# Kernel optimization log

Measured on AMD Instinct MI355X. Metric: run time of the kernel, lower is better.

The kernel has to match this reference:

```python
import jax, jax.numpy as jnp
import numpy as np

L, B, S, E, H, V = 2, 64, 64, 1024, 1024, 32000


def _uni(key, shape, k):
    return jax.random.uniform(key, shape, jnp.float32, -k, k)


def setup_inputs() -> dict:
    key = jax.random.key(0)
    ks = jax.random.split(key, 16)
    k = 1.0 / np.sqrt(H)
    inp = {
        "inputs": jax.random.randint(ks[0], (S, B), 0, V),
        "hidden": jnp.zeros((L, B, H), jnp.float32),
        "emb": jax.random.uniform(ks[1], (V, E), jnp.float32, -0.1, 0.1),
        # per-layer GRU weights stacked on leading L axis (layer0 input = emb = H)
        "Wx": _uni(ks[2], (L, H, H), k),   # linear_W (no bias), used for r gate
        "Ur": _uni(ks[3], (L, H, H), k),
        "br": _uni(ks[4], (L, H), k),
        "Wz": _uni(ks[5], (L, H, H), k),
        "Uz": _uni(ks[6], (L, H, H), k),
        "bz": _uni(ks[7], (L, H), k),
        "Wh": _uni(ks[8], (L, H, H), k),
        "Uh": _uni(ks[9], (L, H, H), k),
        "bh": _uni(ks[10], (L, H), k),
        "dec_W": jax.random.uniform(ks[11], (V, H), jnp.float32, -0.1, 0.1),
        "dec_b": jnp.zeros((V,), jnp.float32),
    }
    return inp


def _gru_cell(x, h, Wx, Ur, br, Wz, Uz, bz, Wh, Uh, bh):
    # faithful to GRU_Hidden.forward (r gate uses linear_W, bias-free W projections)
    r = jax.nn.sigmoid(x @ Wx.T + h @ Ur.T + br)
    z = jax.nn.sigmoid(x @ Wz.T + h @ Uz.T + bz)
    h_cand = jnp.tanh(x @ Wh.T + (r * h) @ Uh.T + bh)
    return (1.0 - z) * h + z * h_cand


def reference(inputs, hidden, emb, Wx, Ur, br, Wz, Uz, bz, Wh, Uh, bh, dec_W, dec_b):
    x_embs = emb[inputs]  # [S, B, E]; dropout is identity (dp_keep_prob = 1.0)
    n_layers = Wx.shape[0]

    def step(h, x_t):
        new_h = []
        inp = x_t
        for l in range(n_layers):
            hl = _gru_cell(inp, h[l], Wx[l], Ur[l], br[l], Wz[l], Uz[l], bz[l], Wh[l], Uh[l], bh[l])
            new_h.append(hl)
            inp = hl
        logits_t = inp @ dec_W.T + dec_b  # [B, V]
        return jnp.stack(new_h), logits_t

    h_final, logits = jax.lax.scan(step, hidden, x_embs)
    return logits, h_final
```

## Files before the change

### kernel.cpp

```cpp
#include <hip/hip_runtime.h>

#define SBV 131072000

typedef __bf16 bf16x8 __attribute__((ext_vector_type(8)));
typedef float  f32x4  __attribute__((ext_vector_type(4)));
typedef unsigned short u16;

__device__ __forceinline__ u16 f2bf(float f) {
  union { float f; unsigned u; } c; c.f = f;
  return (u16)((c.u + 0x7fffu + ((c.u >> 16) & 1u)) >> 16);
}
__device__ __forceinline__ float sigm(float x) { return 1.f / (1.f + __expf(-x)); }
__device__ __forceinline__ float tanh_f(float x) { return 2.f / (1.f + __expf(-2.f * x)) - 1.f; }


__global__ void k_cvtv(const float* __restrict__ src, u16* __restrict__ dst, int n4) {
  const float4* s4 = (const float4*)src;
  ushort4* d4 = (ushort4*)dst;
  for (int i = blockIdx.x * blockDim.x + threadIdx.x; i < n4; i += gridDim.x * blockDim.x) {
    float4 v = s4[i];
    ushort4 o; o.x = f2bf(v.x); o.y = f2bf(v.y); o.z = f2bf(v.z); o.w = f2bf(v.w);
    d4[i] = o;
  }
}

__global__ void k_pack3(const float* __restrict__ sx, const float* __restrict__ sz,
                        const float* __restrict__ sh, int srcOff, u16* __restrict__ dst) {
  int i = blockIdx.x * blockDim.x + threadIdx.x;
  if (i >= 786432) return;
  int g = i >> 18;
  int r4 = i & 262143;
  const float* s = (g == 0 ? sx : (g == 1 ? sz : sh)) + srcOff;
  float4 v = ((const float4*)s)[r4];
  ushort4 o; o.x = f2bf(v.x); o.y = f2bf(v.y); o.z = f2bf(v.z); o.w = f2bf(v.w);
  ((ushort4*)dst)[i] = o;
}

__global__ void k_embed(const int* __restrict__ idx, const float* __restrict__ emb,
                        u16* __restrict__ xe) {
  int i = blockIdx.x * blockDim.x + threadIdx.x;
  if (i >= 1048576) return;
  int row = i >> 8, k4 = i & 255;
  int e = idx[row];
  float4 v = ((const float4*)emb)[(size_t)e * 256 + k4];
  ushort4 o; o.x = f2bf(v.x); o.y = f2bf(v.y); o.z = f2bf(v.z); o.w = f2bf(v.w);
  ((ushort4*)xe)[i] = o;
}

__global__ __launch_bounds__(256) void gemm_bt(const u16* __restrict__ A, const u16* __restrict__ Bm,
                                               float* __restrict__ C, int M, int N, int K, int mtiles) {
  __shared__ u16 As[128 * 32];
  __shared__ u16 Bs[128 * 32];
  const int tid = threadIdx.x;
  const int bm = blockIdx.x % mtiles, bn = blockIdx.x / mtiles;
  const int m0 = bm * 128, n0 = bn * 128;
  const int lane = tid & 63, w = tid >> 6, wm = w & 1, wn = w >> 1;
  const int la = lane & 15, lk = lane >> 4;
  const int srow = tid >> 2, sk = (tid & 3) * 8;
  f32x4 acc[4][4] = {};
  for (int kt = 0; kt < K; kt += 32) {
    const u16* srcA0 = A + (size_t)(m0 + srow) * K + kt + sk;
    const u16* srcA1 = A + (size_t)(m0 + srow + 64) * K + kt + sk;
    const u16* srcB0 = Bm + (size_t)(n0 + srow) * K + kt + sk;
    const u16* srcB1 = Bm + (size_t)(n0 + srow + 64) * K + kt + sk;
    __builtin_amdgcn_global_load_lds((const __attribute__((address_space(1))) void*)srcA0,
        (__attribute__((address_space(3))) void*)((char*)As + tid * 16), 16, 0, 0);
    __builtin_amdgcn_global_load_lds((const __attribute__((address_space(1))) void*)srcA1,
        (__attribute__((address_space(3))) void*)((char*)As + 4096 + tid * 16), 16, 0, 0);
    __builtin_amdgcn_global_load_lds((const __attribute__((address_space(1))) void*)srcB0,
        (__attribute__((address_space(3))) void*)((char*)Bs + tid * 16), 16, 0, 0);
    __builtin_amdgcn_global_load_lds((const __attribute__((address_space(1))) void*)srcB1,
        (__attribute__((address_space(3))) void*)((char*)Bs + 4096 + tid * 16), 16, 0, 0);
    __syncthreads();
    bf16x8 av[4], bv[4];
    #pragma unroll
    for (int m = 0; m < 4; ++m)
      av[m] = *(const bf16x8*)(As + (wm * 64 + m * 16 + la) * 32 + lk * 8);
    #pragma unroll
    for (int n = 0; n < 4; ++n)
      bv[n] = *(const bf16x8*)(Bs + (wn * 64 + n * 16 + la) * 32 + lk * 8);
    #pragma unroll
    for (int m = 0; m < 4; ++m)
      #pragma unroll
      for (int n = 0; n < 4; ++n)
        acc[m][n] = __builtin_amdgcn_mfma_f32_16x16x32_bf16(av[m], bv[n], acc[m][n], 0, 0, 0);
    __syncthreads();
  }
  #pragma unroll
  for (int n = 0; n < 4; ++n) {
    const int gc = n0 + wn * 64 + n * 16 + la;
    #pragma unroll
    for (int m = 0; m < 4; ++m) {
      const int gr0 = m0 + wm * 64 + m * 16 + lk * 4;
      #pragma unroll
      for (int r = 0; r < 4; ++r)
        C[(size_t)(gr0 + r) * N + gc] = acc[m][n][r];
    }
  }
}


__device__ __forceinline__ void waitc1(const unsigned* wptr, unsigned need) {
  if (!need) return;
  unsigned g = 0;
  while (true) {
    unsigned v = need;
    if ((threadIdx.x & 63) == 0)
      asm volatile("global_load_dword %0, %1, off sc1\ns_waitcnt vmcnt(0)"
                   : "=v"(v) : "v"(wptr) : "memory");
    if (__all(v >= need)) break;
    __builtin_amdgcn_s_sleep(1);
    if (++g > 400000u) break;
  }
}

__device__ __forceinline__ void waitc2(const unsigned* w0, unsigned n0,
                                       const unsigned* w1, unsigned n1) {
  unsigned g = 0;
  while (true) {
    const int l = threadIdx.x & 63;
    bool ok = true;
    if (l < 2) {
      const unsigned* p = l ? w1 : w0;
      const unsigned need = l ? n1 : n0;
      unsigned v;
      asm volatile("global_load_dword %0, %1, off sc1\ns_waitcnt vmcnt(0)"
                   : "=v"(v) : "v"(p) : "memory");
      ok = (need == 0) || (v >= need);
    }
    if (__all(ok)) break;
    __builtin_amdgcn_s_sleep(1);
    if (++g > 400000u) break;
  }
}

__device__ __forceinline__ void arrivec(unsigned* wptr, int tid) {
  asm volatile("s_waitcnt vmcnt(0)" ::: "memory");
  __syncthreads();
  if (tid == 0)
    __hip_atomic_fetch_add(wptr, 1u, __ATOMIC_RELAXED, __HIP_MEMORY_SCOPE_AGENT);
}


__global__ __launch_bounds__(256) void k_fused(
    const u16* __restrict__ hinitb,
    const float* __restrict__ hidden,
    const float* __restrict__ X0,
    const u16* __restrict__ Ucat0, const u16* __restrict__ Ucat1,
    const u16* __restrict__ Wcat1,
    const float* __restrict__ br, const float* __restrict__ bz, const float* __restrict__ bh,
    u16* __restrict__ H0seq, u16* __restrict__ H1seq,
    u16* __restrict__ RH0, u16* __restrict__ RH1,
    const u16* __restrict__ decWb,
    const float* __restrict__ decb,
    float* __restrict__ out,
    unsigned* cnt) {
  extern __shared__ char sW[];
  const int tid = threadIdx.x, bid = blockIdx.x;
  const int lane = tid & 63, w = tid >> 6;
  const int la = lane & 15, lk = lane >> 4;

  __builtin_amdgcn_fence(__ATOMIC_ACQUIRE, "agent");

  if (bid >= 128) {
    const int d = bid - 128;
    const int c0 = d * 256 + w * 64;
    const unsigned* cL1 = cnt + 132;
    float bb[4];
    #pragma unroll
    for (int nf = 0; nf < 4; ++nf) bb[nf] = decb[c0 + nf * 16 + la];
    const u16* Bp[4];
    #pragma unroll
    for (int nf = 0; nf < 4; ++nf)
      Bp[nf] = decWb + (size_t)(c0 + nf * 16 + la) * 1024 + lk * 8;
    for (int t = 0; t < 64; ++t) {
      waitc1(cL1 + 2 * t + 2, 64u);
      const u16* Ab = H1seq + (size_t)t * 65536;
      const u16* Ap[4];
      #pragma unroll
      for (int mf = 0; mf < 4; ++mf) Ap[mf] = Ab + (mf * 16 + la) * 1024 + lk * 8;
      f32x4 acc[4][4] = {};
      #pragma unroll 4
      for (int ks = 0; ks < 32; ++ks) {
        bf16x8 av[4], bv[4];
        #pragma unroll
        for (int mf = 0; mf < 4; ++mf) av[mf] = *(const bf16x8*)(Ap[mf] + ks * 32);
        #pragma unroll
        for (int nf = 0; nf < 4; ++nf) bv[nf] = *(const bf16x8*)(Bp[nf] + ks * 32);
        #pragma unroll
        for (int mf = 0; mf < 4; ++mf)
          #pragma unroll
          for (int nf = 0; nf < 4; ++nf)
            acc[mf][nf] = __builtin_amdgcn_mfma_f32_16x16x32_bf16(av[mf], bv[nf], acc[mf][nf], 0, 0, 0);
      }
      #pragma unroll
      for (int mf = 0; mf < 4; ++mf)
        #pragma unroll
        for (int nf = 0; nf < 4; ++nf) {
          const size_t rb = (size_t)(t * 64 + mf * 16 + lk * 4) * 32000 + c0 + nf * 16 + la;
          #pragma unroll
          for (int r = 0; r < 4; ++r)
            out[rb + (size_t)r * 32000] = acc[mf][nf][r] + bb[nf];
        }
    }
    return;
  }

  const int layer = bid >> 6, jb = bid & 63, j0 = jb * 16;
  const int jl = j0 + la;
  const int row0 = w * 16;
  const u16* Ucat = layer ? Ucat1 : Ucat0;
  u16* Hseq = layer ? H1seq : H0seq;
  u16* RHl = layer ? RH1 : RH0;
  const u16* hinit = hinitb + layer * 65536;
  unsigned* cSelf = cnt + layer * 132;
  const unsigned* cL0 = cnt;
  float* houtf = out + (size_t)SBV;

  const int xorv = (la & 7) << 4;
  for (int i = 0; i < 24; ++i) {
    int c = i * 256 + tid;
    int g = c >> 11, rem = c & 2047;
    int urow = rem >> 7, kc = rem & 127;
    uint4 v = *(const uint4*)(Ucat + ((size_t)((g << 10) + j0 + urow)) * 1024 + kc * 8);
    *(uint4*)(sW + (g << 15) + urow * 2048 + ((kc * 16) ^ ((urow & 7) << 4))) = v;
  }
  __syncthreads();
  const char* sWla = sW + la * 2048;

  float h_reg[4], z_reg[4];
  #pragma unroll
  for (int r = 0; r < 4; ++r)
    h_reg[r] = hidden[layer * 65536 + (row0 + lk * 4 + r) * 1024 + jl];
  const float bR = br[layer * 1024 + jl], bZ = bz[layer * 1024 + jl], bH = bh[layer * 1024 + jl];

  const u16* WrR = Wcat1 + (size_t)(j0 + la) * 1024 + lk * 8;
  const u16* WrZ = WrR + (size_t)1024 * 1024;
  const u16* WrH = WrR + (size_t)2048 * 1024;

  for (int t = 0; t < 64; ++t) {
    if (layer == 0) waitc1(cSelf + 2 * t, t ? 64u : 0u);
    else            waitc2(cSelf + 2 * t, t ? 64u : 0u, cL0 + 2 * t + 2, 64u);
    const u16* hsrc = (t == 0) ? hinit : (Hseq + (size_t)(t - 1) * 65536);
    const u16* ap = hsrc + (size_t)(row0 + la) * 1024 + lk * 8;
    f32x4 accR = {0.f, 0.f, 0.f, 0.f}, accZ = {0.f, 0.f, 0.f, 0.f};
    if (layer == 0) {
      #pragma unroll 16
      for (int ks = 0; ks < 32; ++ks) {
        const int kx = (ks * 64 + lk * 16) ^ xorv;
        bf16x8 a = *(const bf16x8*)(ap + ks * 32);
        accR = __builtin_amdgcn_mfma_f32_16x16x32_bf16(a, *(const bf16x8*)(sWla + kx), accR, 0, 0, 0);
        accZ = __builtin_amdgcn_mfma_f32_16x16x32_bf16(a, *(const bf16x8*)(sWla + 32768 + kx), accZ, 0, 0, 0);
      }
    } else {
      const u16* xp = H0seq + (size_t)t * 65536 + (size_t)(row0 + la) * 1024 + lk * 8;
      #pragma unroll 8
      for (int ks = 0; ks < 32; ++ks) {
        const int kx = (ks * 64 + lk * 16) ^ xorv;
        bf16x8 a = *(const bf16x8*)(ap + ks * 32);
        bf16x8 x = *(const bf16x8*)(xp + ks * 32);
        accR = __builtin_amdgcn_mfma_f32_16x16x32_bf16(a, *(const bf16x8*)(sWla + kx), accR, 0, 0, 0);
        accZ = __builtin_amdgcn_mfma_f32_16x16x32_bf16(a, *(const bf16x8*)(sWla + 32768 + kx), accZ, 0, 0, 0);
        accR = __builtin_amdgcn_mfma_f32_16x16x32_bf16(x, *(const bf16x8*)(WrR + ks * 32), accR, 0, 0, 0);
        accZ = __builtin_amdgcn_mfma_f32_16x16x32_bf16(x, *(const bf16x8*)(WrZ + ks * 32), accZ, 0, 0, 0);
      }
    }
    #pragma unroll
    for (int r = 0; r < 4; ++r) {
      const int row = row0 + lk * 4 + r;
      float pr = accR[r] + bR, pz = accZ[r] + bZ;
      if (layer == 0) {
        const float* xf = X0 + (size_t)(t * 64 + row) * 3072 + jl;
        pr += xf[0]; pz += xf[1024];
      }
      float rv = sigm(pr);
      z_reg[r] = sigm(pz);
      unsigned v = f2bf(rv * h_reg[r]);
      u16* p = RHl + (size_t)(t * 64 + row) * 1024 + jl;
      asm volatile("global_store_short %0, %1, off sc1" :: "v"(p), "v"(v));
    }
    arrivec(cSelf + 2 * t + 1, tid);
    waitc1(cSelf + 2 * t + 1, 64u);
    const u16* rp = RHl + (size_t)t * 65536 + (size_t)(row0 + la) * 1024 + lk * 8;
    f32x4 accH = {0.f, 0.f, 0.f, 0.f};
    if (layer == 0) {
      #pragma unroll 16
      for (int ks = 0; ks < 32; ++ks) {
        const int kx = (ks * 64 + lk * 16) ^ xorv;
        bf16x8 a = *(const bf16x8*)(rp + ks * 32);
        accH = __builtin_amdgcn_mfma_f32_16x16x32_bf16(a, *(const bf16x8*)(sWla + 65536 + kx), accH, 0, 0, 0);
      }
    } else {
      const u16* xp = H0seq + (size_t)t * 65536 + (size_t)(row0 + la) * 1024 + lk * 8;
      #pragma unroll 8
      for (int ks = 0; ks < 32; ++ks) {
        const int kx = (ks * 64 + lk * 16) ^ xorv;
        bf16x8 a = *(const bf16x8*)(rp + ks * 32);
        bf16x8 x = *(const bf16x8*)(xp + ks * 32);
        accH = __builtin_amdgcn_mfma_f32_16x16x32_bf16(a, *(const bf16x8*)(sWla + 65536 + kx), accH, 0, 0, 0);
        accH = __builtin_amdgcn_mfma_f32_16x16x32_bf16(x, *(const bf16x8*)(WrH + ks * 32), accH, 0, 0, 0);
      }
    }
    #pragma unroll
    for (int r = 0; r < 4; ++r) {
      const int row = row0 + lk * 4 + r;
      float pre = accH[r] + bH;
      if (layer == 0) pre += X0[(size_t)(t * 64 + row) * 3072 + 2048 + jl];
      float hc = tanh_f(pre);
      float hn = h_reg[r] + z_reg[r] * (hc - h_reg[r]);
      h_reg[r] = hn;
      unsigned v = f2bf(hn);
      u16* p = Hseq + (size_t)(t * 64 + row) * 1024 + jl;
      asm volatile("global_store_short %0, %1, off sc1" :: "v"(p), "v"(v));
      if (t == 63) houtf[layer * 65536 + row * 1024 + jl] = hn;
    }
    arrivec(cSelf + 2 * t + 2, tid);
  }
}

extern "C" void kernel_launch(void* const* d_in, const int* in_sizes, int n_in,
                              void* d_out, int out_size, void* d_ws, size_t ws_size,
                              hipStream_t stream) {
  const int* inputs = (const int*)d_in[0];
  const float* hidden = (const float*)d_in[1];
  const float* emb = (const float*)d_in[2];
  const float* Wx = (const float*)d_in[3];
  const float* Ur = (const float*)d_in[4];
  const float* br = (const float*)d_in[5];
  const float* Wz = (const float*)d_in[6];
  const float* Uz = (const float*)d_in[7];
  const float* bz = (const float*)d_in[8];
  const float* Wh = (const float*)d_in[9];
  const float* Uh = (const float*)d_in[10];
  const float* bh = (const float*)d_in[11];
  const float* decW = (const float*)d_in[12];
  const float* decb = (const float*)d_in[13];
  float* out = (float*)d_out;

  char* ws = (char*)d_ws;
  size_t off = 0;
  auto alloc = [&](size_t bytes) { char* p = ws + off; off += (bytes + 255) & ~(size_t)255; return p; };
  unsigned* cnt = (unsigned*)alloc(4096);
  u16* hinitb = (u16*)alloc((size_t)2 * 64 * 1024 * 2);
  u16* xe     = (u16*)alloc((size_t)4096 * 1024 * 2);
  u16* Wcat0b = (u16*)alloc((size_t)3072 * 1024 * 2);
  u16* Wcat1b = (u16*)alloc((size_t)3072 * 1024 * 2);
  u16* Ucat0b = (u16*)alloc((size_t)3072 * 1024 * 2);
  u16* Ucat1b = (u16*)alloc((size_t)3072 * 1024 * 2);
  u16* decWb  = (u16*)alloc((size_t)32000 * 1024 * 2);
  float* X0   = (float*)alloc((size_t)4096 * 3072 * 4);
  u16* H0seq  = (u16*)alloc((size_t)4096 * 1024 * 2);
  u16* H1seq  = (u16*)alloc((size_t)4096 * 1024 * 2);
  u16* RH0    = (u16*)alloc((size_t)4096 * 1024 * 2);
  u16* RH1    = (u16*)alloc((size_t)4096 * 1024 * 2);

  hipMemsetAsync(cnt, 0, 4096, stream);
  k_cvtv<<<128, 256, 0, stream>>>(hidden, hinitb, 32768);
  k_pack3<<<3072, 256, 0, stream>>>(Wx, Wz, Wh, 0, Wcat0b);
  k_pack3<<<3072, 256, 0, stream>>>(Wx, Wz, Wh, 1048576, Wcat1b);
  k_pack3<<<3072, 256, 0, stream>>>(Ur, Uz, Uh, 0, Ucat0b);
  k_pack3<<<3072, 256, 0, stream>>>(Ur, Uz, Uh, 1048576, Ucat1b);
  k_embed<<<4096, 256, 0, stream>>>(inputs, emb, xe);
  k_cvtv<<<4096, 256, 0, stream>>>(decW, decWb, 8192000);

  gemm_bt<<<768, 256, 0, stream>>>(xe, Wcat0b, X0, 4096, 3072, 1024, 32);

  (void)hipFuncSetAttribute(reinterpret_cast<const void*>(&k_fused),
                            hipFuncAttributeMaxDynamicSharedMemorySize, 98304);
  k_fused<<<253, 256, 98304, stream>>>(hinitb, hidden, X0, Ucat0b, Ucat1b, Wcat1b,
                                       br, bz, bh, H0seq, H1seq, RH0, RH1,
                                       decWb, decb, out, cnt);
}
```

Before: 2.650 ms.

## Replace atomic block counters with per-wave stamp flags and prefetch X0 before waits

Replaces the per-layer atomic counters and block-wide __syncthreads barrier with per-wave stamp arrays. Each wave writes its step number to its own slot, and waiting waves poll all 64 producer slots in parallel, one lane per slot, without sleeping. This removes the block barrier and atomic contention from the serial recurrence's critical path, so each wave only waits on the row group it actually consumes. X0 input-projection loads are also issued before the waits so their latency overlaps the spin. The trade-off is more polling traffic from busy-spinning and a correctness dependence on per-wave memory ordering.

```diff
diff --git a/kernel.cpp b/kernel.cpp
--- a/kernel.cpp
+++ b/kernel.cpp
@@ -100,45 +100,55 @@
 }
 
 
-__device__ __forceinline__ void waitc1(const unsigned* wptr, unsigned need) {
-  if (!need) return;
+__device__ __forceinline__ void waitS(const unsigned* st, unsigned tgt, int lane) {
+  if (!tgt) return;
   unsigned g = 0;
   while (true) {
-    unsigned v = need;
-    if ((threadIdx.x & 63) == 0)
-      asm volatile("global_load_dword %0, %1, off sc1\ns_waitcnt vmcnt(0)"
-                   : "=v"(v) : "v"(wptr) : "memory");
-    if (__all(v >= need)) break;
-    __builtin_amdgcn_s_sleep(1);
-    if (++g > 400000u) break;
-  }
-}
-
-__device__ __forceinline__ void waitc2(const unsigned* w0, unsigned n0,
-                                       const unsigned* w1, unsigned n1) {
+    unsigned v;
+    asm volatile("global_load_dword %0, %1, off sc1\ns_waitcnt vmcnt(0)"
+                 : "=v"(v) : "v"(st + lane) : "memory");
+    if (__all(v >= tgt)) break;
+    if (++g > 150000u) break;
+  }
+}
+
+__device__ __forceinline__ void waitS2(const unsigned* s0, unsigned t0,
+                                       const unsigned* s1, unsigned t1, int lane) {
   unsigned g = 0;
   while (true) {
-    const int l = threadIdx.x & 63;
-    bool ok = true;
-    if (l < 2) {
-      const unsigned* p = l ? w1 : w0;
-      const unsigned need = l ? n1 : n0;
-      unsigned v;
-      asm volatile("global_load_dword %0, %1, off sc1\ns_waitcnt vmcnt(0)"
-                   : "=v"(v) : "v"(p) : "memory");
-      ok = (need == 0) || (v >= need);
-    }
-    if (__all(ok)) break;
+    unsigned v0 = t0, v1;
+    if (t0)
+      asm volatile("global_load_dword %0, %1, off sc1" : "=v"(v0) : "v"(s0 + lane) : "memory");
+    asm volatile("global_load_dword %0, %1, off sc1\ns_waitcnt vmcnt(0)"
+                 : "=v"(v1) : "v"(s1 + lane) : "memory");
+    if (__all(v0 >= t0 && v1 >= t1)) break;
+    if (++g > 150000u) break;
+  }
+}
+
+__device__ __forceinline__ void arriveW(unsigned* p, unsigned val, int lane) {
+  asm volatile("s_waitcnt vmcnt(0)" ::: "memory");
+  if (lane == 0)
+    asm volatile("global_store_dword %0, %1, off sc1" :: "v"(p), "v"(val) : "memory");
+}
+
+__device__ __forceinline__ void waitDec(const unsigned* stL1, unsigned tgt, int lane) {
+  unsigned g = 0;
+  while (true) {
+    unsigned a, b, c, d;
+    asm volatile("global_load_dword %0, %4, off sc1\n"
+                 "global_load_dword %1, %5, off sc1\n"
+                 "global_load_dword %2, %6, off sc1\n"
+                 "global_load_dword %3, %7, off sc1\n"
+                 "s_waitcnt vmcnt(0)"
+                 : "=v"(a), "=v"(b), "=v"(c), "=v"(d)
+                 : "v"(stL1 + lane), "v"(stL1 + 64 + lane),
+                   "v"(stL1 + 128 + lane), "v"(stL1 + 192 + lane)
+                 : "memory");
+    if (__all(a >= tgt && b >= tgt && c >= tgt && d >= tgt)) break;
     __builtin_amdgcn_s_sleep(1);
-    if (++g > 400000u) break;
-  }
-}
-
-__device__ __forceinline__ void arrivec(unsigned* wptr, int tid) {
-  asm volatile("s_waitcnt vmcnt(0)" ::: "memory");
-  __syncthreads();
-  if (tid == 0)
-    __hip_atomic_fetch_add(wptr, 1u, __ATOMIC_RELAXED, __HIP_MEMORY_SCOPE_AGENT);
+    if (++g > 300000u) break;
+  }
 }
 
 
@@ -154,7 +164,7 @@
     const u16* __restrict__ decWb,
     const float* __restrict__ decb,
     float* __restrict__ out,
-    unsigned* cnt) {
+    unsigned* stamp) {
   extern __shared__ char sW[];
   const int tid = threadIdx.x, bid = blockIdx.x;
   const int lane = tid & 63, w = tid >> 6;
@@ -165,7 +175,7 @@
   if (bid >= 128) {
     const int d = bid - 128;
     const int c0 = d * 256 + w * 64;
-    const unsigned* cL1 = cnt + 132;
+    const unsigned* stL1 = stamp + 4 * 64;
     float bb[4];
     #pragma unroll
     for (int nf = 0; nf < 4; ++nf) bb[nf] = decb[c0 + nf * 16 + la];
@@ -174,7 +184,7 @@
     for (int nf = 0; nf < 4; ++nf)
       Bp[nf] = decWb + (size_t)(c0 + nf * 16 + la) * 1024 + lk * 8;
     for (int t = 0; t < 64; ++t) {
-      waitc1(cL1 + 2 * t + 2, 64u);
+      waitDec(stL1, 2 * t + 2, lane);
       const u16* Ab = H1seq + (size_t)t * 65536;
       const u16* Ap[4];
       #pragma unroll
@@ -213,8 +223,9 @@
   u16* Hseq = layer ? H1seq : H0seq;
   u16* RHl = layer ? RH1 : RH0;
   const u16* hinit = hinitb + layer * 65536;
-  unsigned* cSelf = cnt + layer * 132;
-  const unsigned* cL0 = cnt;
+  unsigned* stSelfW = stamp + (layer * 4 + w) * 64 + jb;
+  const unsigned* stSelf = stamp + (layer * 4 + w) * 64;
+  const unsigned* stL0   = stamp + w * 64;
   float* houtf = out + (size_t)SBV;
 
   const int xorv = (la & 7) << 4;
@@ -239,8 +250,16 @@
   const u16* WrH = WrR + (size_t)2048 * 1024;
 
   for (int t = 0; t < 64; ++t) {
-    if (layer == 0) waitc1(cSelf + 2 * t, t ? 64u : 0u);
-    else            waitc2(cSelf + 2 * t, t ? 64u : 0u, cL0 + 2 * t + 2, 64u);
+    float xfr[4], xfz[4];
+    if (layer == 0) {
+      #pragma unroll
+      for (int r = 0; r < 4; ++r) {
+        const float* xf = X0 + (size_t)(t * 64 + row0 + lk * 4 + r) * 3072 + jl;
+        xfr[r] = xf[0]; xfz[r] = xf[1024];
+      }
+    }
+    if (layer == 0) waitS(stSelf, 2 * t, lane);
+    else            waitS2(stSelf, 2 * t, stL0, 2 * t + 2, lane);
     const u16* hsrc = (t == 0) ? hinit : (Hseq + (size_t)(t - 1) * 65536);
     const u16* ap = hsrc + (size_t)(row0 + la) * 1024 + lk * 8;
     f32x4 accR = {0.f, 0.f, 0.f, 0.f}, accZ = {0.f, 0.f, 0.f, 0.f};
@@ -269,18 +288,21 @@
     for (int r = 0; r < 4; ++r) {
       const int row = row0 + lk * 4 + r;
       float pr = accR[r] + bR, pz = accZ[r] + bZ;
-      if (layer == 0) {
-        const float* xf = X0 + (size_t)(t * 64 + row) * 3072 + jl;
-        pr += xf[0]; pz += xf[1024];
-      }
+      if (layer == 0) { pr += xfr[r]; pz += xfz[r]; }
       float rv = sigm(pr);
       z_reg[r] = sigm(pz);
       unsigned v = f2bf(rv * h_reg[r]);
       u16* p = RHl + (size_t)(t * 64 + row) * 1024 + jl;
       asm volatile("global_store_short %0, %1, off sc1" :: "v"(p), "v"(v));
     }
-    arrivec(cSelf + 2 * t + 1, tid);
-    waitc1(cSelf + 2 * t + 1, 64u);
+    arriveW(stSelfW, 2 * t + 1, lane);
+    float xfh[4];
+    if (layer == 0) {
+      #pragma unroll
+      for (int r = 0; r < 4; ++r)
+        xfh[r] = X0[(size_t)(t * 64 + row0 + lk * 4 + r) * 3072 + 2048 + jl];
+    }
+    waitS(stSelf, 2 * t + 1, lane);
     const u16* rp = RHl + (size_t)t * 65536 + (size_t)(row0 + la) * 1024 + lk * 8;
     f32x4 accH = {0.f, 0.f, 0.f, 0.f};
     if (layer == 0) {
@@ -305,7 +327,7 @@
     for (int r = 0; r < 4; ++r) {
       const int row = row0 + lk * 4 + r;
       float pre = accH[r] + bH;
-      if (layer == 0) pre += X0[(size_t)(t * 64 + row) * 3072 + 2048 + jl];
+      if (layer == 0) pre += xfh[r];
       float hc = tanh_f(pre);
       float hn = h_reg[r] + z_reg[r] * (hc - h_reg[r]);
       h_reg[r] = hn;
@@ -314,7 +336,7 @@
       asm volatile("global_store_short %0, %1, off sc1" :: "v"(p), "v"(v));
       if (t == 63) houtf[layer * 65536 + row * 1024 + jl] = hn;
     }
-    arrivec(cSelf + 2 * t + 2, tid);
+    arriveW(stSelfW, 2 * t + 2, lane);
   }
 }
 
@@ -340,7 +362,7 @@
   char* ws = (char*)d_ws;
   size_t off = 0;
   auto alloc = [&](size_t bytes) { char* p = ws + off; off += (bytes + 255) & ~(size_t)255; return p; };
-  unsigned* cnt = (unsigned*)alloc(4096);
+  unsigned* stamp = (unsigned*)alloc(4096);
   u16* hinitb = (u16*)alloc((size_t)2 * 64 * 1024 * 2);
   u16* xe     = (u16*)alloc((size_t)4096 * 1024 * 2);
   u16* Wcat0b = (u16*)alloc((size_t)3072 * 1024 * 2);
@@ -354,7 +376,7 @@
   u16* RH0    = (u16*)alloc((size_t)4096 * 1024 * 2);
   u16* RH1    = (u16*)alloc((size_t)4096 * 1024 * 2);
 
-  hipMemsetAsync(cnt, 0, 4096, stream);
+  hipMemsetAsync(stamp, 0, 4096, stream);
   k_cvtv<<<128, 256, 0, stream>>>(hidden, hinitb, 32768);
   k_pack3<<<3072, 256, 0, stream>>>(Wx, Wz, Wh, 0, Wcat0b);
   k_pack3<<<3072, 256, 0, stream>>>(Wx, Wz, Wh, 1048576, Wcat1b);
@@ -369,5 +391,5 @@
                             hipFuncAttributeMaxDynamicSharedMemorySize, 98304);
   k_fused<<<253, 256, 98304, stream>>>(hinitb, hidden, X0, Ucat0b, Ucat1b, Wcat1b,
                                        br, bz, bh, H0seq, H1seq, RH0, RH1,
-                                       decWb, decb, out, cnt);
-}
+                                       decWb, decb, out, stamp);
+}
```

After: 2.639 ms. No clear change (-0.4%).
